# Performance work log

Hardware: AMD Instinct MI355X
Metric: run time of the kernel (lower is better)

Reference implementation:

```python
import jax, jax.numpy as jnp
import numpy as np

D_MODEL = 1024
NUM_HEAD = 16
D_HEAD = 64


def setup_inputs() -> dict:
    key = jax.random.key(0)
    ks = jax.random.split(key, 9)
    b, p = 8, 1024
    s = 1.0 / np.sqrt(D_MODEL)
    inp = {
        "x": jax.random.normal(ks[0], (b, p, D_MODEL), jnp.float32),
        "w_q": jax.random.uniform(ks[1], (D_MODEL, D_MODEL), jnp.float32, -s, s),
        "b_q": jax.random.uniform(ks[2], (D_MODEL,), jnp.float32, -s, s),
        "w_k": jax.random.uniform(ks[3], (D_MODEL, D_MODEL), jnp.float32, -s, s),
        "b_k": jax.random.uniform(ks[4], (D_MODEL,), jnp.float32, -s, s),
        "w_v": jax.random.uniform(ks[5], (D_MODEL, D_MODEL), jnp.float32, -s, s),
        "b_v": jax.random.uniform(ks[6], (D_MODEL,), jnp.float32, -s, s),
        "w_o": jax.random.uniform(ks[7], (D_MODEL, D_MODEL), jnp.float32, -s, s),
        "b_o": jax.random.uniform(ks[8], (D_MODEL,), jnp.float32, -s, s),
    }
    return inp


def reference(x, w_q, b_q, w_k, b_k, w_v, b_v, w_o, b_o):
    b, p, _ = x.shape
    # projections (torch Linear: y = x @ W.T + b; here weights stored [in,out])
    q = x @ w_q + b_q
    k = x @ w_k + b_k
    v = x @ w_v + b_v
    # [b, h, p, d]
    q = q.reshape(b, p, NUM_HEAD, D_HEAD).transpose(0, 2, 1, 3)
    k = k.reshape(b, p, NUM_HEAD, D_HEAD).transpose(0, 2, 1, 3)
    v = v.reshape(b, p, NUM_HEAD, D_HEAD).transpose(0, 2, 1, 3)
    scale = 1.0 / np.sqrt(D_HEAD).astype(np.float32)
    scores = jnp.einsum("bhqd,bhkd->bhqk", q, k) * scale
    attn = jax.nn.softmax(scores, axis=-1)
    out = jnp.einsum("bhqk,bhkd->bhqd", attn, v)
    out = out.transpose(0, 2, 1, 3).reshape(b, p, D_MODEL)
    return out @ w_o + b_o
```

## Files before the change

### kernel.cpp

```cpp
#include <hip/hip_runtime.h>
#include <stdint.h>


typedef __attribute__((ext_vector_type(8))) short short8;
typedef __attribute__((ext_vector_type(4))) short s16x4;
typedef __attribute__((ext_vector_type(4))) float f32x4;

__device__ __forceinline__ short f2bf(float f) {
  unsigned u = __builtin_bit_cast(unsigned, f);
  u += 0x7fffu + ((u >> 16) & 1u);
  return (short)(u >> 16);
}

__device__ __forceinline__ unsigned pk2bf(float a, float b) {
  unsigned ua = __builtin_bit_cast(unsigned, a);
  unsigned ub = __builtin_bit_cast(unsigned, b);
  ua += 0x7fffu + ((ua >> 16) & 1u);
  ub += 0x7fffu + ((ub >> 16) & 1u);
  return (ua >> 16) | (ub & 0xffff0000u);
}

typedef __attribute__((address_space(3))) void lds_void;
typedef __attribute__((address_space(1))) void gbl_void;
#define GLD16(gp, lp) \
  __builtin_amdgcn_global_load_lds((gbl_void*)(gp), (lds_void*)(lp), 16, 0, 0)

#define MFMA(a, b, c) __builtin_amdgcn_mfma_f32_16x16x32_bf16((a), (b), (c), 0, 0, 0)

__global__ __launch_bounds__(256) void k_convert(const float* __restrict__ src,
                                                 short* __restrict__ dst) {
  int i = (blockIdx.x * 256 + threadIdx.x) * 8;
  const float4* s = (const float4*)(src + i);
  float4 f0 = s[0], f1 = s[1];
  short8 o;
  o[0] = f2bf(f0.x); o[1] = f2bf(f0.y); o[2] = f2bf(f0.z); o[3] = f2bf(f0.w);
  o[4] = f2bf(f1.x); o[5] = f2bf(f1.y); o[6] = f2bf(f1.z); o[7] = f2bf(f1.w);
  *(short8*)(dst + i) = o;
}

__global__ __launch_bounds__(256) void k_transpose4(const float* __restrict__ s0,
                                                    const float* __restrict__ s1,
                                                    const float* __restrict__ s2,
                                                    const float* __restrict__ s3,
                                                    short* __restrict__ d0,
                                                    short* __restrict__ d1,
                                                    short* __restrict__ d2,
                                                    short* __restrict__ d3) {
  __shared__ float tile[32][33];
  const float* srcs[4] = {s0, s1, s2, s3};
  short* dsts[4] = {d0, d1, d2, d3};
  const float* src = srcs[blockIdx.z];
  short* dst = dsts[blockIdx.z];
  int tx = threadIdx.x, ty = threadIdx.y;
  int x0 = blockIdx.x * 32, y0 = blockIdx.y * 32;
#pragma unroll
  for (int i = 0; i < 32; i += 8)
    tile[ty + i][tx] = src[(y0 + ty + i) * 1024 + x0 + tx];
  __syncthreads();
#pragma unroll
  for (int i = 0; i < 32; i += 8)
    dst[(x0 + ty + i) * 1024 + y0 + tx] = f2bf(tile[tx][ty + i]);
}

template <int MODE>
__global__ __launch_bounds__(256, 3) void k_gemm(const short* __restrict__ A,
                                                 const short* __restrict__ Bt,
                                                 const float* __restrict__ bias0,
                                                 const float* __restrict__ bias1,
                                                 const float* __restrict__ bias2,
                                                 short* __restrict__ o0,
                                                 short* __restrict__ o1,
                                                 short* __restrict__ o2,
                                                 float* __restrict__ of) {
  __shared__ __align__(16) short a_lds[128 * 64];
  __shared__ __align__(16) short b_lds[128 * 64];
  const int tid = threadIdx.x;
  const int m0 = blockIdx.y * 128;
  const int n0 = blockIdx.x * 128;
  const int w = tid >> 6;
  const int lane = tid & 63;
  const int ll = lane & 15;
  const int qd = lane >> 4;
  const int wm = (w & 1) * 64;
  const int wn = (w >> 1) * 64;

  const int srow = tid >> 3;
  const int schunk = ((tid & 7) ^ (srow & 7)) * 8;
  const short* ag = A + (long)(m0 + srow) * 1024 + schunk;
  const short* bg = Bt + (long)(n0 + srow) * 1024 + schunk;

  f32x4 acc[4][4] = {};

  for (int kt = 0; kt < 1024; kt += 64) {
#pragma unroll
    for (int j = 0; j < 4; ++j) {
      GLD16(ag + j * 32768 + kt, &a_lds[j * 2048 + tid * 8]);
      GLD16(bg + j * 32768 + kt, &b_lds[j * 2048 + tid * 8]);
    }
    __syncthreads();
#pragma unroll
    for (int kh = 0; kh < 2; ++kh) {
      const int xoff = (((kh * 4 + qd) ^ (ll & 7)) * 8);
      short8 af[4], bfr[4];
#pragma unroll
      for (int mt = 0; mt < 4; ++mt)
        af[mt] = *(const short8*)&a_lds[(wm + mt * 16 + ll) * 64 + xoff];
#pragma unroll
      for (int nt = 0; nt < 4; ++nt)
        bfr[nt] = *(const short8*)&b_lds[(wn + nt * 16 + ll) * 64 + xoff];
#pragma unroll
      for (int mt = 0; mt < 4; ++mt)
#pragma unroll
        for (int nt = 0; nt < 4; ++nt)
          acc[mt][nt] = MFMA(af[mt], bfr[nt], acc[mt][nt]);
    }
    __syncthreads();
  }

  if (MODE == 0) {
#pragma unroll
    for (int nt = 0; nt < 4; ++nt) {
      int n = n0 + wn + nt * 16 + ll;
      int which = n >> 10;
      int nl = n & 1023;
      int h = nl >> 6, d = n & 63;
      if (which == 2) {
        float bv = bias2[nl];
        const int b = m0 >> 10;
        const int p0 = (m0 & 1023) + wm;
#pragma unroll
        for (int mt = 0; mt < 4; ++mt) {
          int p = p0 + mt * 16 + qd * 4;
          int2 pk;
          pk.x = (int)pk2bf(acc[mt][nt][0] + bv, acc[mt][nt][1] + bv);
          pk.y = (int)pk2bf(acc[mt][nt][2] + bv, acc[mt][nt][3] + bv);
          *(int2*)&o2[(long)(b * 16 + h) * 65536 + d * 1024 + p] = pk;
        }
      } else {
        float bv = (which == 0) ? bias0[nl] : bias1[nl];
        float sc = (which == 0) ? 0.125f : 1.0f;
        short* o = (which == 0) ? o0 : o1;
#pragma unroll
        for (int mt = 0; mt < 4; ++mt) {
#pragma unroll
          for (int r = 0; r < 4; ++r) {
            int m = m0 + wm + mt * 16 + qd * 4 + r;
            int b = m >> 10, p = m & 1023;
            o[(long)(b * 16 + h) * 65536 + p * 64 + d] = f2bf((acc[mt][nt][r] + bv) * sc);
          }
        }
      }
    }
  } else {
#pragma unroll
    for (int nt = 0; nt < 4; ++nt) {
      int n = n0 + wn + nt * 16 + ll;
      float bv = bias0[n];
#pragma unroll
      for (int mt = 0; mt < 4; ++mt) {
#pragma unroll
        for (int r = 0; r < 4; ++r) {
          int m = m0 + wm + mt * 16 + qd * 4 + r;
          of[(long)m * 1024 + n] = acc[mt][nt][r] + bv;
        }
      }
    }
  }
}

__global__ __launch_bounds__(256, 4) void k_attn(const short* __restrict__ Q,
                                                 const short* __restrict__ K,
                                                 const short* __restrict__ VT,
                                                 short* __restrict__ O) {
  __shared__ __align__(16) short k_lds[4096];
  __shared__ __align__(16) short vt_lds[4096];
  __shared__ __align__(16) short p_lds[4][32 * 72];
  const int tid = threadIdx.x;
  const int w = tid >> 6, lane = tid & 63, ll = lane & 15, qd = lane >> 4;
  const int bh = blockIdx.y, qb = blockIdx.x;
  const long hoff = (long)bh * 65536;
  const int qr0 = qb * 128 + w * 32;

  const short* qg = Q + hoff + (long)(qr0 + ll) * 64 + qd * 8;
  short8 qf[2][2];
  qf[0][0] = *(const short8*)qg;
  qf[0][1] = *(const short8*)(qg + 32);
  qf[1][0] = *(const short8*)(qg + 1024);
  qf[1][1] = *(const short8*)(qg + 1024 + 32);

  const int sr = tid >> 3;
  const int swz = (tid & 7) ^ (sr & 7);
  const short* kg = K + hoff + sr * 64 + swz * 8;
  const short* vg = VT + hoff + (long)sr * 1024 + swz * 8;
  short* kl0 = &k_lds[tid * 8];
  short* kl1 = &k_lds[2048 + tid * 8];
  short* vl0 = &vt_lds[tid * 8];
  short* vl1 = &vt_lds[2048 + tid * 8];

  const int swzr = ll & 7;
  const int fro0 = ll * 64 + ((qd ^ swzr) * 8);
  const int fro1 = ll * 64 + (((4 + qd) ^ swzr) * 8);
  short* pw = &p_lds[w][0];

  f32x4 oacc[2][4] = {};
  float l_part[2] = {0.f, 0.f};

  for (int c = 0; c < 16; ++c) {
    GLD16(kg + c * 4096, kl0);
    GLD16(kg + c * 4096 + 2048, kl1);
    GLD16(vg + c * 64, vl0);
    GLD16(vg + c * 64 + 32768, vl1);
    __syncthreads();

    f32x4 s[2][4];
#pragma unroll
    for (int jt = 0; jt < 4; ++jt) {
      short8 kf0 = *(const short8*)&k_lds[jt * 1024 + fro0];
      short8 kf1 = *(const short8*)&k_lds[jt * 1024 + fro1];
      f32x4 t0 = {};
      t0 = MFMA(kf0, qf[0][0], t0);
      t0 = MFMA(kf1, qf[0][1], t0);
      s[0][jt] = t0;
      f32x4 t1 = {};
      t1 = MFMA(kf0, qf[1][0], t1);
      t1 = MFMA(kf1, qf[1][1], t1);
      s[1][jt] = t1;
    }

    short8 pf[2][2];
#pragma unroll
    for (int g = 0; g < 2; ++g) {
      float rs = 0.f;
#pragma unroll
      for (int jt = 0; jt < 4; ++jt)
#pragma unroll
        for (int r = 0; r < 4; ++r) {
          float e = __expf(s[g][jt][r]);
          s[g][jt][r] = e;
          rs += e;
        }
      l_part[g] += rs;
      short* pg = pw + (g * 16 + ll) * 72;
#pragma unroll
      for (int jt = 0; jt < 4; ++jt) {
        int2 pk;
        pk.x = (int)pk2bf(s[g][jt][0], s[g][jt][1]);
        pk.y = (int)pk2bf(s[g][jt][2], s[g][jt][3]);
        *(int2*)&pg[jt * 16 + qd * 4] = pk;
      }
      pf[g][0] = *(const short8*)&pg[qd * 8];
      pf[g][1] = *(const short8*)&pg[32 + qd * 8];
    }

#pragma unroll
    for (int dt = 0; dt < 4; ++dt) {
      short8 vf0 = *(const short8*)&vt_lds[dt * 1024 + fro0];
      short8 vf1 = *(const short8*)&vt_lds[dt * 1024 + fro1];
      oacc[0][dt] = MFMA(vf0, pf[0][0], oacc[0][dt]);
      oacc[0][dt] = MFMA(vf1, pf[0][1], oacc[0][dt]);
      oacc[1][dt] = MFMA(vf0, pf[1][0], oacc[1][dt]);
      oacc[1][dt] = MFMA(vf1, pf[1][1], oacc[1][dt]);
    }
    __syncthreads();
  }

  const int b = bh >> 4, h = bh & 15;
#pragma unroll
  for (int g = 0; g < 2; ++g) {
    float l = l_part[g];
    l += __shfl_xor(l, 16, 64);
    l += __shfl_xor(l, 32, 64);
    const float inv = 1.0f / l;
    const long row = (long)(b * 1024 + qr0 + g * 16 + ll);
#pragma unroll
    for (int dt = 0; dt < 4; ++dt) {
      int2 ov;
      ov.x = (int)pk2bf(oacc[g][dt][0] * inv, oacc[g][dt][1] * inv);
      ov.y = (int)pk2bf(oacc[g][dt][2] * inv, oacc[g][dt][3] * inv);
      *(int2*)&O[row * 1024 + h * 64 + dt * 16 + qd * 4] = ov;
    }
  }
}

extern "C" void kernel_launch(void* const* d_in, const int* in_sizes, int n_in,
                              void* d_out, int out_size, void* d_ws, size_t ws_size,
                              hipStream_t stream) {
  const float* x   = (const float*)d_in[0];
  const float* w_q = (const float*)d_in[1];
  const float* b_q = (const float*)d_in[2];
  const float* w_k = (const float*)d_in[3];
  const float* b_k = (const float*)d_in[4];
  const float* w_v = (const float*)d_in[5];
  const float* b_v = (const float*)d_in[6];
  const float* w_o = (const float*)d_in[7];
  const float* b_o = (const float*)d_in[8];

  char* ws = (char*)d_ws;
  short* xb    = (short*)(ws);
  short* wqkvT = (short*)(ws + (16ull << 20));
  short* woT   = (short*)(ws + (22ull << 20));
  short* qw    = (short*)(ws + (24ull << 20));
  short* kw    = (short*)(ws + (40ull << 20));
  short* vw    = (short*)(ws + (56ull << 20));

  k_convert<<<4096, 256, 0, stream>>>(x, xb);
  k_transpose4<<<dim3(32, 32, 4), dim3(32, 8), 0, stream>>>(
      w_q, w_k, w_v, w_o, wqkvT, wqkvT + (1 << 20), wqkvT + (2 << 20), woT);

  k_gemm<0><<<dim3(24, 64), 256, 0, stream>>>(xb, wqkvT, b_q, b_k, b_v,
                                              qw, kw, vw, nullptr);

  k_attn<<<dim3(8, 128), 256, 0, stream>>>(qw, kw, vw, xb);

  k_gemm<1><<<dim3(8, 64), 256, 0, stream>>>(xb, woT, b_o, nullptr, nullptr,
                                             nullptr, nullptr, nullptr, (float*)d_out);
}
```

Measured before the change: 242.4 us.

## Split attention keys across waves with LDS reduction; fuse input prep kernels

The x-to-bf16 conversion and the four weight transposes now run as one launch, removing a kernel launch. The attention kernel is reorganised so each block handles 64 query rows and each wave takes a quarter of the key range. K and V fragments are read straight from global memory instead of being staged through LDS. Partial outputs and row sums are reduced across waves through LDS at the end. This drops the per-chunk block barriers and doubles the grid, at the cost of uncoalesced global fragment loads, more accumulator registers and an extra reduction phase.

```diff
diff --git a/kernel.cpp b/kernel.cpp
--- a/kernel.cpp
+++ b/kernel.cpp
@@ -27,25 +27,31 @@
 
 #define MFMA(a, b, c) __builtin_amdgcn_mfma_f32_16x16x32_bf16((a), (b), (c), 0, 0, 0)
 
-__global__ __launch_bounds__(256) void k_convert(const float* __restrict__ src,
-                                                 short* __restrict__ dst) {
-  int i = (blockIdx.x * 256 + threadIdx.x) * 8;
-  const float4* s = (const float4*)(src + i);
-  float4 f0 = s[0], f1 = s[1];
-  short8 o;
-  o[0] = f2bf(f0.x); o[1] = f2bf(f0.y); o[2] = f2bf(f0.z); o[3] = f2bf(f0.w);
-  o[4] = f2bf(f1.x); o[5] = f2bf(f1.y); o[6] = f2bf(f1.z); o[7] = f2bf(f1.w);
-  *(short8*)(dst + i) = o;
-}
-
-__global__ __launch_bounds__(256) void k_transpose4(const float* __restrict__ s0,
-                                                    const float* __restrict__ s1,
-                                                    const float* __restrict__ s2,
-                                                    const float* __restrict__ s3,
-                                                    short* __restrict__ d0,
-                                                    short* __restrict__ d1,
-                                                    short* __restrict__ d2,
-                                                    short* __restrict__ d3) {
+__global__ __launch_bounds__(256) void k_prep(const float* __restrict__ x,
+                                              short* __restrict__ xb,
+                                              const float* __restrict__ s0,
+                                              const float* __restrict__ s1,
+                                              const float* __restrict__ s2,
+                                              const float* __restrict__ s3,
+                                              short* __restrict__ d0,
+                                              short* __restrict__ d1,
+                                              short* __restrict__ d2,
+                                              short* __restrict__ d3) {
+  if (blockIdx.z == 4) {
+    int t = threadIdx.y * 32 + threadIdx.x;
+    int bid = blockIdx.y * 32 + blockIdx.x;
+#pragma unroll
+    for (int j = 0; j < 4; ++j) {
+      int i = (bid * 1024 + j * 256 + t) * 8;
+      const float4* s = (const float4*)(x + i);
+      float4 f0 = s[0], f1 = s[1];
+      short8 o;
+      o[0] = f2bf(f0.x); o[1] = f2bf(f0.y); o[2] = f2bf(f0.z); o[3] = f2bf(f0.w);
+      o[4] = f2bf(f1.x); o[5] = f2bf(f1.y); o[6] = f2bf(f1.z); o[7] = f2bf(f1.w);
+      *(short8*)(xb + i) = o;
+    }
+    return;
+  }
   __shared__ float tile[32][33];
   const float* srcs[4] = {s0, s1, s2, s3};
   short* dsts[4] = {d0, d1, d2, d3};
@@ -168,117 +174,106 @@
   }
 }
 
-__global__ __launch_bounds__(256, 4) void k_attn(const short* __restrict__ Q,
+__global__ __launch_bounds__(256, 3) void k_attn(const short* __restrict__ Q,
                                                  const short* __restrict__ K,
                                                  const short* __restrict__ VT,
                                                  short* __restrict__ O) {
-  __shared__ __align__(16) short k_lds[4096];
-  __shared__ __align__(16) short vt_lds[4096];
-  __shared__ __align__(16) short p_lds[4][32 * 72];
+  __shared__ __align__(16) char lds[17408];
   const int tid = threadIdx.x;
   const int w = tid >> 6, lane = tid & 63, ll = lane & 15, qd = lane >> 4;
   const int bh = blockIdx.y, qb = blockIdx.x;
   const long hoff = (long)bh * 65536;
-  const int qr0 = qb * 128 + w * 32;
-
-  const short* qg = Q + hoff + (long)(qr0 + ll) * 64 + qd * 8;
-  short8 qf[2][2];
-  qf[0][0] = *(const short8*)qg;
-  qf[0][1] = *(const short8*)(qg + 32);
-  qf[1][0] = *(const short8*)(qg + 1024);
-  qf[1][1] = *(const short8*)(qg + 1024 + 32);
-
-  const int sr = tid >> 3;
-  const int swz = (tid & 7) ^ (sr & 7);
-  const short* kg = K + hoff + sr * 64 + swz * 8;
-  const short* vg = VT + hoff + (long)sr * 1024 + swz * 8;
-  short* kl0 = &k_lds[tid * 8];
-  short* kl1 = &k_lds[2048 + tid * 8];
-  short* vl0 = &vt_lds[tid * 8];
-  short* vl1 = &vt_lds[2048 + tid * 8];
-
-  const int swzr = ll & 7;
-  const int fro0 = ll * 64 + ((qd ^ swzr) * 8);
-  const int fro1 = ll * 64 + (((4 + qd) ^ swzr) * 8);
-  short* pw = &p_lds[w][0];
-
-  f32x4 oacc[2][4] = {};
-  float l_part[2] = {0.f, 0.f};
-
-  for (int c = 0; c < 16; ++c) {
-    GLD16(kg + c * 4096, kl0);
-    GLD16(kg + c * 4096 + 2048, kl1);
-    GLD16(vg + c * 64, vl0);
-    GLD16(vg + c * 64 + 32768, vl1);
-    __syncthreads();
-
-    f32x4 s[2][4];
+  const int qr0 = qb * 64;
+
+  short* pw = (short*)(lds + w * 2304);
+  const short* Qb = Q + hoff + (long)(qr0 + ll) * 64 + qd * 8;
+  const short* Kb = K + hoff + (long)ll * 64 + qd * 8;
+  const short* Vb = VT + hoff + (long)ll * 1024 + qd * 8;
+
+  f32x4 oacc[4][4] = {};
+  float l_part[4] = {0.f, 0.f, 0.f, 0.f};
+
+#pragma unroll
+  for (int i = 0; i < 4; ++i) {
+    const int ck = (w + i * 4) * 64;
+    short8 kf[4][2];
 #pragma unroll
     for (int jt = 0; jt < 4; ++jt) {
-      short8 kf0 = *(const short8*)&k_lds[jt * 1024 + fro0];
-      short8 kf1 = *(const short8*)&k_lds[jt * 1024 + fro1];
-      f32x4 t0 = {};
-      t0 = MFMA(kf0, qf[0][0], t0);
-      t0 = MFMA(kf1, qf[0][1], t0);
-      s[0][jt] = t0;
-      f32x4 t1 = {};
-      t1 = MFMA(kf0, qf[1][0], t1);
-      t1 = MFMA(kf1, qf[1][1], t1);
-      s[1][jt] = t1;
-    }
-
-    short8 pf[2][2];
-#pragma unroll
-    for (int g = 0; g < 2; ++g) {
+      const short* kp = Kb + (long)(ck + jt * 16) * 64;
+      kf[jt][0] = *(const short8*)kp;
+      kf[jt][1] = *(const short8*)(kp + 32);
+    }
+#pragma unroll
+    for (int g = 0; g < 4; ++g) {
+      const short* qp = Qb + g * 1024;
+      short8 q0 = *(const short8*)qp;
+      short8 q1 = *(const short8*)(qp + 32);
       float rs = 0.f;
 #pragma unroll
-      for (int jt = 0; jt < 4; ++jt)
-#pragma unroll
-        for (int r = 0; r < 4; ++r) {
-          float e = __expf(s[g][jt][r]);
-          s[g][jt][r] = e;
-          rs += e;
-        }
+      for (int jt = 0; jt < 4; ++jt) {
+        f32x4 t = {};
+        t = MFMA(kf[jt][0], q0, t);
+        t = MFMA(kf[jt][1], q1, t);
+        float e0 = __expf(t[0]), e1 = __expf(t[1]);
+        float e2 = __expf(t[2]), e3 = __expf(t[3]);
+        rs += (e0 + e1) + (e2 + e3);
+        int2 pk;
+        pk.x = (int)pk2bf(e0, e1);
+        pk.y = (int)pk2bf(e2, e3);
+        *(int2*)&pw[ll * 72 + jt * 16 + qd * 4] = pk;
+      }
       l_part[g] += rs;
-      short* pg = pw + (g * 16 + ll) * 72;
-#pragma unroll
-      for (int jt = 0; jt < 4; ++jt) {
-        int2 pk;
-        pk.x = (int)pk2bf(s[g][jt][0], s[g][jt][1]);
-        pk.y = (int)pk2bf(s[g][jt][2], s[g][jt][3]);
-        *(int2*)&pg[jt * 16 + qd * 4] = pk;
-      }
-      pf[g][0] = *(const short8*)&pg[qd * 8];
-      pf[g][1] = *(const short8*)&pg[32 + qd * 8];
-    }
-
-#pragma unroll
-    for (int dt = 0; dt < 4; ++dt) {
-      short8 vf0 = *(const short8*)&vt_lds[dt * 1024 + fro0];
-      short8 vf1 = *(const short8*)&vt_lds[dt * 1024 + fro1];
-      oacc[0][dt] = MFMA(vf0, pf[0][0], oacc[0][dt]);
-      oacc[0][dt] = MFMA(vf1, pf[0][1], oacc[0][dt]);
-      oacc[1][dt] = MFMA(vf0, pf[1][0], oacc[1][dt]);
-      oacc[1][dt] = MFMA(vf1, pf[1][1], oacc[1][dt]);
-    }
-    __syncthreads();
-  }
-
-  const int b = bh >> 4, h = bh & 15;
-#pragma unroll
-  for (int g = 0; g < 2; ++g) {
+      short8 pf0 = *(const short8*)&pw[ll * 72 + qd * 8];
+      short8 pf1 = *(const short8*)&pw[ll * 72 + 32 + qd * 8];
+#pragma unroll
+      for (int dt = 0; dt < 4; ++dt) {
+        const short* vp = Vb + (long)dt * 16384 + ck;
+        short8 v0 = *(const short8*)vp;
+        short8 v1 = *(const short8*)(vp + 32);
+        oacc[g][dt] = MFMA(v0, pf0, oacc[g][dt]);
+        oacc[g][dt] = MFMA(v1, pf1, oacc[g][dt]);
+      }
+    }
+  }
+
+  float* l_red = (float*)(lds + 16384);
+#pragma unroll
+  for (int g = 0; g < 4; ++g) {
     float l = l_part[g];
     l += __shfl_xor(l, 16, 64);
     l += __shfl_xor(l, 32, 64);
-    const float inv = 1.0f / l;
-    const long row = (long)(b * 1024 + qr0 + g * 16 + ll);
-#pragma unroll
-    for (int dt = 0; dt < 4; ++dt) {
-      int2 ov;
-      ov.x = (int)pk2bf(oacc[g][dt][0] * inv, oacc[g][dt][1] * inv);
-      ov.y = (int)pk2bf(oacc[g][dt][2] * inv, oacc[g][dt][3] * inv);
-      *(int2*)&O[row * 1024 + h * 64 + dt * 16 + qd * 4] = ov;
-    }
+    if (qd == 0) l_red[(w * 4 + g) * 16 + ll] = l;
+  }
+  __syncthreads();
+
+  float* R = (float*)lds;
+  const int b = bh >> 4, h = bh & 15;
+  for (int dt = 0; dt < 4; ++dt) {
+#pragma unroll
+    for (int g = 0; g < 4; ++g)
+      *(f32x4*)&R[((w * 4 + g) * 64 + lane) * 4] = oacc[g][dt];
+    __syncthreads();
+    if (w == dt) {
+#pragma unroll
+      for (int g = 0; g < 4; ++g) {
+        f32x4 sum = oacc[g][dt];
+#pragma unroll
+        for (int v = 0; v < 4; ++v)
+          if (v != w) {
+            f32x4 o = *(const f32x4*)&R[((v * 4 + g) * 64 + lane) * 4];
+            sum = sum + o;
+          }
+        float lt = l_red[(0 + g) * 16 + ll] + l_red[(4 + g) * 16 + ll] +
+                   l_red[(8 + g) * 16 + ll] + l_red[(12 + g) * 16 + ll];
+        float inv = 1.0f / lt;
+        long row = (long)(b * 1024 + qr0 + g * 16 + ll);
+        int2 ov;
+        ov.x = (int)pk2bf(sum[0] * inv, sum[1] * inv);
+        ov.y = (int)pk2bf(sum[2] * inv, sum[3] * inv);
+        *(int2*)&O[row * 1024 + h * 64 + dt * 16 + qd * 4] = ov;
+      }
+    }
+    __syncthreads();
   }
 }
 
@@ -303,14 +298,14 @@
   short* kw    = (short*)(ws + (40ull << 20));
   short* vw    = (short*)(ws + (56ull << 20));
 
-  k_convert<<<4096, 256, 0, stream>>>(x, xb);
-  k_transpose4<<<dim3(32, 32, 4), dim3(32, 8), 0, stream>>>(
-      w_q, w_k, w_v, w_o, wqkvT, wqkvT + (1 << 20), wqkvT + (2 << 20), woT);
+  k_prep<<<dim3(32, 32, 5), dim3(32, 8), 0, stream>>>(
+      x, xb, w_q, w_k, w_v, w_o,
+      wqkvT, wqkvT + (1 << 20), wqkvT + (2 << 20), woT);
 
   k_gemm<0><<<dim3(24, 64), 256, 0, stream>>>(xb, wqkvT, b_q, b_k, b_v,
                                               qw, kw, vw, nullptr);
 
-  k_attn<<<dim3(8, 128), 256, 0, stream>>>(qw, kw, vw, xb);
+  k_attn<<<dim3(16, 128), 256, 0, stream>>>(qw, kw, vw, xb);
 
   k_gemm<1><<<dim3(8, 64), 256, 0, stream>>>(xb, woT, b_o, nullptr, nullptr,
                                              nullptr, nullptr, nullptr, (float*)d_out);
```

Result: slower. 453.5 us (+87.1%).
